# Performance work log

Hardware: AMD Instinct MI355X
Metric: run time of the kernel (lower is better)

The kernel has to match this reference:

```python
import jax, jax.numpy as jnp
import numpy as np

B, N, F_IN, F_OUT = 8, 2048, 128, 128


def setup_inputs() -> dict:
    key = jax.random.key(0)
    k1, k2, k3, k4 = jax.random.split(key, 4)
    h = jax.random.normal(k1, (B, N, F_IN), dtype=jnp.float32)
    adj = (jax.random.uniform(k2, (B, N, N)) > 0.5).astype(jnp.float32)
    adj = jnp.maximum(adj, jnp.eye(N, dtype=jnp.float32)[None])
    # torch nn.Linear weights: W is [out_features, in_features], a is [1, 2*out_features]
    W = jax.random.normal(k3, (F_OUT, F_IN), dtype=jnp.float32) * 0.05
    a = jax.random.normal(k4, (1, 2 * F_OUT), dtype=jnp.float32) * 0.05
    return {"h": h, "adj": adj, "W": W, "a": a}


def reference(h, adj, W, a):
    # Wh = W(h): [B, N, F_OUT]
    Wh = jnp.einsum("bnf,of->bno", h, W)
    # attn_fc(concat(Wh_i, Wh_j)) == (Wh_i @ a1) + (Wh_j @ a2): exact split of the
    # linear layer, avoiding the O(B*N*N*2F) concat intermediate.
    a1 = a[0, :F_OUT]
    a2 = a[0, F_OUT:]
    e_i = Wh @ a1  # [B, N]  score contribution of destination node i
    e_j = Wh @ a2  # [B, N]  score contribution of source node j
    e = e_i[:, :, None] + e_j[:, None, :]  # [B, N, N]
    e = e + (1.0 - adj) * (-1e9)
    alpha = jax.nn.softmax(e, axis=-1)  # [B, N, N]
    # weighted aggregation: h_out[b,i] = sum_j alpha[b,i,j] * Wh[b,j]
    h_out = jnp.einsum("bij,bjo->bio", alpha, Wh)
    return h_out
```

## Files before the change

### kernel.cpp

```cpp
#include <hip/hip_runtime.h>
#include <stdint.h>

#define AS1 __attribute__((address_space(1)))
#define AS3 __attribute__((address_space(3)))

typedef __bf16 bf16x8 __attribute__((ext_vector_type(8)));
typedef float f32x4 __attribute__((ext_vector_type(4)));

constexpr int NB = 8;
constexpr int N  = 2048;
constexpr int F  = 128;
constexpr size_t NSL = (size_t)NB * N * F;
constexpr size_t DSL = (size_t)NB * N;

__device__ __forceinline__ unsigned short bf16r(float f) {
    unsigned u = __float_as_uint(f);
    return (unsigned short)((u + 0x7FFFu + ((u >> 16) & 1u)) >> 16);
}
__device__ __forceinline__ float bf2f(unsigned short s) {
    return __uint_as_float(((unsigned)s) << 16);
}


__global__ __launch_bounds__(256) void k1_wh(const float* __restrict__ h,
                                             const float* __restrict__ W,
                                             const float* __restrict__ a,
                                             unsigned short* __restrict__ Wb2,
                                             unsigned short* __restrict__ p16) {
    __shared__ float epart[2][64];

    const int tid  = threadIdx.x;
    const int lane = tid & 63, wid = tid >> 6;
    const int quad = lane >> 4, l15 = lane & 15;
    const int wm = wid >> 1, wn = wid & 1;
    const int m0 = blockIdx.x * 64;
    const int batch = m0 >> 11;
    const int nbase = m0 & 2047;

    f32x4 acc[2][4] = {};

#pragma unroll
    for (int kk = 0; kk < 4; ++kk) {
        const int k = kk * 32 + quad * 8;
        bf16x8 afr[2], bfr[4];
#pragma unroll
        for (int rt = 0; rt < 2; ++rt) {
            const float* src = h + (size_t)(m0 + wm * 32 + rt * 16 + l15) * F + k;
            float4 x0 = *(const float4*)src;
            float4 x1 = *(const float4*)(src + 4);
            afr[rt][0] = (__bf16)x0.x; afr[rt][1] = (__bf16)x0.y;
            afr[rt][2] = (__bf16)x0.z; afr[rt][3] = (__bf16)x0.w;
            afr[rt][4] = (__bf16)x1.x; afr[rt][5] = (__bf16)x1.y;
            afr[rt][6] = (__bf16)x1.z; afr[rt][7] = (__bf16)x1.w;
        }
#pragma unroll
        for (int ct = 0; ct < 4; ++ct) {
            const int o = wn * 64 + ct * 16 + l15;
            const float* src = W + (size_t)o * F + k;
            float4 x0 = *(const float4*)src;
            float4 x1 = *(const float4*)(src + 4);
            bfr[ct][0] = (__bf16)x0.x; bfr[ct][1] = (__bf16)x0.y;
            bfr[ct][2] = (__bf16)x0.z; bfr[ct][3] = (__bf16)x0.w;
            bfr[ct][4] = (__bf16)x1.x; bfr[ct][5] = (__bf16)x1.y;
            bfr[ct][6] = (__bf16)x1.z; bfr[ct][7] = (__bf16)x1.w;
        }
#pragma unroll
        for (int rt = 0; rt < 2; ++rt)
#pragma unroll
            for (int ct = 0; ct < 4; ++ct)
                acc[rt][ct] = __builtin_amdgcn_mfma_f32_16x16x32_bf16(
                    afr[rt], bfr[ct], acc[rt][ct], 0, 0, 0);
    }

    float a2v[4];
#pragma unroll
    for (int ct = 0; ct < 4; ++ct) a2v[ct] = a[F + wn * 64 + ct * 16 + l15];

    float ep[2][4];
#pragma unroll
    for (int rt = 0; rt < 2; ++rt)
#pragma unroll
        for (int g = 0; g < 4; ++g) {
            float s = 0.f;
#pragma unroll
            for (int ct = 0; ct < 4; ++ct) s += acc[rt][ct][g] * a2v[ct];
            ep[rt][g] = s;
        }
#pragma unroll
    for (int m = 1; m < 16; m <<= 1)
#pragma unroll
        for (int rt = 0; rt < 2; ++rt)
#pragma unroll
            for (int g = 0; g < 4; ++g)
                ep[rt][g] += __shfl_xor(ep[rt][g], m);

    if (l15 == 0)
#pragma unroll
        for (int rt = 0; rt < 2; ++rt)
#pragma unroll
            for (int g = 0; g < 4; ++g)
                epart[wn][wm * 32 + rt * 16 + quad * 4 + g] = ep[rt][g];
    __syncthreads();

#pragma unroll
    for (int rt = 0; rt < 2; ++rt)
#pragma unroll
        for (int ct = 0; ct < 4; ++ct) {
            const int o  = wn * 64 + ct * 16 + l15;
            const int r0 = wm * 32 + rt * 16 + quad * 4;
            const int n0 = nbase + r0;
            ushort4 v;
#pragma unroll
            for (int g = 0; g < 4; ++g) {
                const float e  = epart[0][r0 + g] + epart[1][r0 + g];
                const float pf = bf2f(bf16r(expf(e)));
                (&v.x)[g] = bf16r(pf * acc[rt][ct][g]);
            }
            size_t off = (size_t)batch * N * F + (size_t)(n0 >> 3) * 1024 + o * 8 + (n0 & 7);
            *(ushort4*)&Wb2[off] = v;
        }

    if (tid < 64) {
        const float e = epart[0][tid] + epart[1][tid];
        p16[batch * N + nbase + tid] = bf16r(expf(e));
    }
}

__global__ __launch_bounds__(256) void k3_attn(const float* __restrict__ adj,
                                               const unsigned short* __restrict__ Wb2,
                                               const unsigned short* __restrict__ p16,
                                               unsigned short* __restrict__ nump,
                                               float* __restrict__ denp) {
    __shared__ __align__(16) float          At[2][64 * 32];
    __shared__ __align__(16) unsigned short Bt[2][4 * 1024];
    __shared__ __align__(16) unsigned short Pt[512];

    const int tid  = threadIdx.x;
    const int lane = tid & 63, wid = tid >> 6;
    const int quad = lane >> 4, l15 = lane & 15;
    const int wm = wid >> 1, wn = wid & 1;
    const int b  = blockIdx.x & 7;
    const int r  = blockIdx.x >> 3;
    const int it = r >> 2, jq = r & 3;
    const int i0 = it * 64, j0 = jq * 512;

    const float* aSrcs[2];
#pragma unroll
    for (int s = 0; s < 2; ++s) {
        const int ri = (wid * 2 + s) * 8 + (lane >> 3);
        aSrcs[s] = adj + (size_t)b * N * N + (size_t)(i0 + ri) * N + j0
                 + (((lane & 7) ^ (ri & 7)) << 2);
    }
    const char* bSrc = (const char*)Wb2 + (size_t)b * N * F * 2
                     + (size_t)jq * 131072 + (size_t)wid * 2048 + lane * 16;
    const char* pSrc = (const char*)p16 + ((size_t)b * N + j0) * 2 + lane * 16;

    auto stage = [&](int buf, int c) {
#pragma unroll
        for (int s = 0; s < 2; ++s)
            __builtin_amdgcn_global_load_lds((const AS1 void*)(aSrcs[s] + c * 32),
                (AS3 void*)((char*)&At[buf][0] + (wid * 2 + s) * 1024), 16, 0, 0);
#pragma unroll
        for (int s = 0; s < 2; ++s)
            __builtin_amdgcn_global_load_lds(
                (const AS1 void*)(bSrc + (size_t)c * 8192 + s * 1024),
                (AS3 void*)((char*)&Bt[buf][0] + wid * 2048 + s * 1024), 16, 0, 0);
    };

    f32x4 acc[2][4] = {};
    f32x4 dacc[2] = {};

    if (wid == 0)
        __builtin_amdgcn_global_load_lds((const AS1 void*)pSrc,
            (AS3 void*)((char*)&Pt[0]), 16, 0, 0);
    stage(0, 0);

    for (int c = 0; c < 16; ++c) {
        const int cur = c & 1;
        __syncthreads();
        if (c + 1 < 16) stage(cur ^ 1, c + 1);

        const char* aB = (const char*)&At[cur][0];
        bf16x8 pv = *(const bf16x8*)((const char*)&Pt[0] + c * 64 + quad * 16);

        bf16x8 af[2];
#pragma unroll
        for (int rt = 0; rt < 2; ++rt) {
            const int row = wm * 32 + rt * 16 + l15;
            const int s0 = (quad * 2)     ^ (row & 7);
            const int s1 = (quad * 2 + 1) ^ (row & 7);
            f32x4 x0 = *(const f32x4*)(aB + row * 128 + (s0 << 4));
            f32x4 x1 = *(const f32x4*)(aB + row * 128 + (s1 << 4));
            af[rt][0] = (__bf16)x0[0]; af[rt][1] = (__bf16)x0[1];
            af[rt][2] = (__bf16)x0[2]; af[rt][3] = (__bf16)x0[3];
            af[rt][4] = (__bf16)x1[0]; af[rt][5] = (__bf16)x1[1];
            af[rt][6] = (__bf16)x1[2]; af[rt][7] = (__bf16)x1[3];
        }
#pragma unroll
        for (int ct = 0; ct < 4; ++ct) {
            const char* bb = (const char*)&Bt[cur][0]
                           + quad * 2048 + wn * 1024 + ct * 256 + l15 * 16;
            bf16x8 bf = *(const bf16x8*)bb;
#pragma unroll
            for (int rt = 0; rt < 2; ++rt)
                acc[rt][ct] = __builtin_amdgcn_mfma_f32_16x16x32_bf16(
                    af[rt], bf, acc[rt][ct], 0, 0, 0);
        }
#pragma unroll
        for (int rt = 0; rt < 2; ++rt)
            dacc[rt] = __builtin_amdgcn_mfma_f32_16x16x32_bf16(
                af[rt], pv, dacc[rt], 0, 0, 0);
    }

    unsigned short* np = nump + (size_t)jq * NSL + (size_t)b * N * F;
#pragma unroll
    for (int rt = 0; rt < 2; ++rt)
#pragma unroll
        for (int ct = 0; ct < 4; ++ct) {
            const int o = wn * 64 + ct * 16 + l15;
#pragma unroll
            for (int g = 0; g < 4; ++g) {
                const int i = i0 + wm * 32 + rt * 16 + quad * 4 + g;
                np[(size_t)i * F + o] = bf16r(acc[rt][ct][g]);
            }
        }
    float* dp = denp + (size_t)jq * DSL + (size_t)b * N;
#pragma unroll
    for (int rt = 0; rt < 2; ++rt)
#pragma unroll
        for (int g = 0; g < 4; ++g)
            if (l15 == quad * 4 + g)
                dp[i0 + wm * 32 + rt * 16 + quad * 4 + g] = dacc[rt][g];
}

__global__ __launch_bounds__(256) void k4_reduce(const unsigned short* __restrict__ nump,
                                                 const float* __restrict__ denp,
                                                 float* __restrict__ out) {
    const int b   = blockIdx.x & 7;
    const int row = (blockIdx.x >> 3) * 8 + (threadIdx.x >> 5);
    const int o4  = (threadIdx.x & 31) * 4;
    const size_t base = ((size_t)b * N + row) * F + o4;

    float s0 = 0.f, s1 = 0.f, s2 = 0.f, s3 = 0.f, d = 0.f;
#pragma unroll
    for (int q = 0; q < 4; ++q) {
        ushort4 v = *(const ushort4*)&nump[q * NSL + base];
        s0 += bf2f(v.x); s1 += bf2f(v.y); s2 += bf2f(v.z); s3 += bf2f(v.w);
        d  += denp[q * DSL + (size_t)b * N + row];
    }
    const float inv = 1.0f / d;
    f32x4 o = { s0 * inv, s1 * inv, s2 * inv, s3 * inv };
    *(f32x4*)&out[base] = o;
}

extern "C" void kernel_launch(void* const* d_in, const int* in_sizes, int n_in,
                              void* d_out, int out_size, void* d_ws, size_t ws_size,
                              hipStream_t stream) {
    const float* h   = (const float*)d_in[0];
    const float* adj = (const float*)d_in[1];
    const float* W   = (const float*)d_in[2];
    const float* a   = (const float*)d_in[3];
    float* out = (float*)d_out;

    unsigned short* Wb2  = (unsigned short*)d_ws;
    unsigned short* p16  = (unsigned short*)((char*)d_ws + (4u << 20));
    unsigned short* nump = (unsigned short*)((char*)d_ws + (8u << 20));
    float*          denp = (float*)((char*)d_ws + (24u << 20));

    k1_wh<<<NB * N / 64, 256, 0, stream>>>(h, W, a, Wb2, p16);
    k3_attn<<<NB * 32 * 4, 256, 0, stream>>>(adj, Wb2, p16, nump, denp);
    k4_reduce<<<NB * N / 8, 256, 0, stream>>>(nump, denp, out);
}
```

Before: 221.6 us.

## Fuse attention and reduction into one kernel without split-K partials

Replaces the split-K attention kernel and separate reduction kernel with a single kernel that computes the full j-range per block. It normalizes by the denominator and writes fp32 output directly. Operands now come straight from global memory into registers with one-step software prefetch instead of LDS double buffering. This drops the partial-sum round trip and a launch, but cuts the grid to 512 blocks, lengthens each block's serial loop, and loses LDS reuse of Wb2 tiles across waves.

```diff
diff --git a/kernel.cpp b/kernel.cpp
--- a/kernel.cpp
+++ b/kernel.cpp
@@ -10,8 +10,6 @@
 constexpr int NB = 8;
 constexpr int N  = 2048;
 constexpr int F  = 128;
-constexpr size_t NSL = (size_t)NB * N * F;
-constexpr size_t DSL = (size_t)NB * N;
 
 __device__ __forceinline__ unsigned short bf16r(float f) {
     unsigned u = __float_as_uint(f);
@@ -126,131 +124,73 @@
     }
 }
 
-__global__ __launch_bounds__(256) void k3_attn(const float* __restrict__ adj,
-                                               const unsigned short* __restrict__ Wb2,
-                                               const unsigned short* __restrict__ p16,
-                                               unsigned short* __restrict__ nump,
-                                               float* __restrict__ denp) {
-    __shared__ __align__(16) float          At[2][64 * 32];
-    __shared__ __align__(16) unsigned short Bt[2][4 * 1024];
-    __shared__ __align__(16) unsigned short Pt[512];
-
+__global__ __launch_bounds__(256, 2) void k3_fused(const float* __restrict__ adj,
+                                                   const unsigned short* __restrict__ Wb2,
+                                                   const unsigned short* __restrict__ p16,
+                                                   float* __restrict__ out) {
     const int tid  = threadIdx.x;
     const int lane = tid & 63, wid = tid >> 6;
     const int quad = lane >> 4, l15 = lane & 15;
     const int wm = wid >> 1, wn = wid & 1;
     const int b  = blockIdx.x & 7;
-    const int r  = blockIdx.x >> 3;
-    const int it = r >> 2, jq = r & 3;
-    const int i0 = it * 64, j0 = jq * 512;
-
-    const float* aSrcs[2];
-#pragma unroll
-    for (int s = 0; s < 2; ++s) {
-        const int ri = (wid * 2 + s) * 8 + (lane >> 3);
-        aSrcs[s] = adj + (size_t)b * N * N + (size_t)(i0 + ri) * N + j0
-                 + (((lane & 7) ^ (ri & 7)) << 2);
-    }
-    const char* bSrc = (const char*)Wb2 + (size_t)b * N * F * 2
-                     + (size_t)jq * 131072 + (size_t)wid * 2048 + lane * 16;
-    const char* pSrc = (const char*)p16 + ((size_t)b * N + j0) * 2 + lane * 16;
-
-    auto stage = [&](int buf, int c) {
-#pragma unroll
-        for (int s = 0; s < 2; ++s)
-            __builtin_amdgcn_global_load_lds((const AS1 void*)(aSrcs[s] + c * 32),
-                (AS3 void*)((char*)&At[buf][0] + (wid * 2 + s) * 1024), 16, 0, 0);
-#pragma unroll
-        for (int s = 0; s < 2; ++s)
-            __builtin_amdgcn_global_load_lds(
-                (const AS1 void*)(bSrc + (size_t)c * 8192 + s * 1024),
-                (AS3 void*)((char*)&Bt[buf][0] + wid * 2048 + s * 1024), 16, 0, 0);
-    };
-
-    f32x4 acc[2][4] = {};
-    f32x4 dacc[2] = {};
-
-    if (wid == 0)
-        __builtin_amdgcn_global_load_lds((const AS1 void*)pSrc,
-            (AS3 void*)((char*)&Pt[0]), 16, 0, 0);
-    stage(0, 0);
-
-    for (int c = 0; c < 16; ++c) {
-        const int cur = c & 1;
-        __syncthreads();
-        if (c + 1 < 16) stage(cur ^ 1, c + 1);
-
-        const char* aB = (const char*)&At[cur][0];
-        bf16x8 pv = *(const bf16x8*)((const char*)&Pt[0] + c * 64 + quad * 16);
-
-        bf16x8 af[2];
-#pragma unroll
-        for (int rt = 0; rt < 2; ++rt) {
-            const int row = wm * 32 + rt * 16 + l15;
-            const int s0 = (quad * 2)     ^ (row & 7);
-            const int s1 = (quad * 2 + 1) ^ (row & 7);
-            f32x4 x0 = *(const f32x4*)(aB + row * 128 + (s0 << 4));
-            f32x4 x1 = *(const f32x4*)(aB + row * 128 + (s1 << 4));
-            af[rt][0] = (__bf16)x0[0]; af[rt][1] = (__bf16)x0[1];
-            af[rt][2] = (__bf16)x0[2]; af[rt][3] = (__bf16)x0[3];
-            af[rt][4] = (__bf16)x1[0]; af[rt][5] = (__bf16)x1[1];
-            af[rt][6] = (__bf16)x1[2]; af[rt][7] = (__bf16)x1[3];
-        }
-#pragma unroll
-        for (int ct = 0; ct < 4; ++ct) {
-            const char* bb = (const char*)&Bt[cur][0]
-                           + quad * 2048 + wn * 1024 + ct * 256 + l15 * 16;
-            bf16x8 bf = *(const bf16x8*)bb;
-#pragma unroll
-            for (int rt = 0; rt < 2; ++rt)
-                acc[rt][ct] = __builtin_amdgcn_mfma_f32_16x16x32_bf16(
-                    af[rt], bf, acc[rt][ct], 0, 0, 0);
-        }
-#pragma unroll
-        for (int rt = 0; rt < 2; ++rt)
-            dacc[rt] = __builtin_amdgcn_mfma_f32_16x16x32_bf16(
-                af[rt], pv, dacc[rt], 0, 0, 0);
-    }
-
-    unsigned short* np = nump + (size_t)jq * NSL + (size_t)b * N * F;
-#pragma unroll
-    for (int rt = 0; rt < 2; ++rt)
-#pragma unroll
-        for (int ct = 0; ct < 4; ++ct) {
-            const int o = wn * 64 + ct * 16 + l15;
-#pragma unroll
-            for (int g = 0; g < 4; ++g) {
-                const int i = i0 + wm * 32 + rt * 16 + quad * 4 + g;
-                np[(size_t)i * F + o] = bf16r(acc[rt][ct][g]);
-            }
-        }
-    float* dp = denp + (size_t)jq * DSL + (size_t)b * N;
-#pragma unroll
-    for (int rt = 0; rt < 2; ++rt)
-#pragma unroll
-        for (int g = 0; g < 4; ++g)
-            if (l15 == quad * 4 + g)
-                dp[i0 + wm * 32 + rt * 16 + quad * 4 + g] = dacc[rt][g];
-}
-
-__global__ __launch_bounds__(256) void k4_reduce(const unsigned short* __restrict__ nump,
-                                                 const float* __restrict__ denp,
-                                                 float* __restrict__ out) {
-    const int b   = blockIdx.x & 7;
-    const int row = (blockIdx.x >> 3) * 8 + (threadIdx.x >> 5);
-    const int o4  = (threadIdx.x & 31) * 4;
-    const size_t base = ((size_t)b * N + row) * F + o4;
-
-    float s0 = 0.f, s1 = 0.f, s2 = 0.f, s3 = 0.f, d = 0.f;
-#pragma unroll
-    for (int q = 0; q < 4; ++q) {
-        ushort4 v = *(const ushort4*)&nump[q * NSL + base];
-        s0 += bf2f(v.x); s1 += bf2f(v.y); s2 += bf2f(v.z); s3 += bf2f(v.w);
-        d  += denp[q * DSL + (size_t)b * N + row];
-    }
-    const float inv = 1.0f / d;
-    f32x4 o = { s0 * inv, s1 * inv, s2 * inv, s3 * inv };
-    *(f32x4*)&out[base] = o;
+    const int it = blockIdx.x >> 3;
+    const int i0 = it * 32;
+    const int rowA = i0 + wm * 16 + l15;
+
+    const float* aP = adj + (size_t)b * N * N + (size_t)rowA * N + quad * 8;
+    const char*  bP = (const char*)Wb2 + (size_t)b * (N * F * 2)
+                    + quad * 2048 + wn * 1024 + l15 * 16;
+    const char*  pP = (const char*)p16 + (size_t)b * N * 2 + quad * 16;
+
+    f32x4 acc[4] = {};
+    f32x4 dacc = {0.f, 0.f, 0.f, 0.f};
+
+    f32x4  a0n = *(const f32x4*)(aP);
+    f32x4  a1n = *(const f32x4*)(aP + 4);
+    bf16x8 bn0 = *(const bf16x8*)(bP + 0 * 256);
+    bf16x8 bn1 = *(const bf16x8*)(bP + 1 * 256);
+    bf16x8 bn2 = *(const bf16x8*)(bP + 2 * 256);
+    bf16x8 bn3 = *(const bf16x8*)(bP + 3 * 256);
+    bf16x8 pn  = *(const bf16x8*)(pP);
+
+#pragma unroll 2
+    for (int c = 0; c < 64; ++c) {
+        f32x4  a0 = a0n, a1 = a1n;
+        bf16x8 b0 = bn0, b1 = bn1, b2 = bn2, b3 = bn3, pv = pn;
+        if (c + 1 < 64) {
+            const float* aN = aP + (size_t)(c + 1) * 32;
+            const char*  bN = bP + (size_t)(c + 1) * 8192;
+            a0n = *(const f32x4*)(aN);
+            a1n = *(const f32x4*)(aN + 4);
+            bn0 = *(const bf16x8*)(bN + 0 * 256);
+            bn1 = *(const bf16x8*)(bN + 1 * 256);
+            bn2 = *(const bf16x8*)(bN + 2 * 256);
+            bn3 = *(const bf16x8*)(bN + 3 * 256);
+            pn  = *(const bf16x8*)(pP + (size_t)(c + 1) * 64);
+        }
+        bf16x8 af;
+        af[0] = (__bf16)a0[0]; af[1] = (__bf16)a0[1];
+        af[2] = (__bf16)a0[2]; af[3] = (__bf16)a0[3];
+        af[4] = (__bf16)a1[0]; af[5] = (__bf16)a1[1];
+        af[6] = (__bf16)a1[2]; af[7] = (__bf16)a1[3];
+
+        acc[0] = __builtin_amdgcn_mfma_f32_16x16x32_bf16(af, b0, acc[0], 0, 0, 0);
+        acc[1] = __builtin_amdgcn_mfma_f32_16x16x32_bf16(af, b1, acc[1], 0, 0, 0);
+        acc[2] = __builtin_amdgcn_mfma_f32_16x16x32_bf16(af, b2, acc[2], 0, 0, 0);
+        acc[3] = __builtin_amdgcn_mfma_f32_16x16x32_bf16(af, b3, acc[3], 0, 0, 0);
+        dacc   = __builtin_amdgcn_mfma_f32_16x16x32_bf16(af, pv, dacc,   0, 0, 0);
+    }
+
+#pragma unroll
+    for (int g = 0; g < 4; ++g) {
+        const float inv = 1.0f / dacc[g];
+        float* orow = out + ((size_t)b * N + i0 + wm * 16 + quad * 4 + g) * F
+                    + wn * 64 + l15;
+        orow[0]  = acc[0][g] * inv;
+        orow[16] = acc[1][g] * inv;
+        orow[32] = acc[2][g] * inv;
+        orow[48] = acc[3][g] * inv;
+    }
 }
 
 extern "C" void kernel_launch(void* const* d_in, const int* in_sizes, int n_in,
@@ -262,12 +202,9 @@
     const float* a   = (const float*)d_in[3];
     float* out = (float*)d_out;
 
-    unsigned short* Wb2  = (unsigned short*)d_ws;
-    unsigned short* p16  = (unsigned short*)((char*)d_ws + (4u << 20));
-    unsigned short* nump = (unsigned short*)((char*)d_ws + (8u << 20));
-    float*          denp = (float*)((char*)d_ws + (24u << 20));
+    unsigned short* Wb2 = (unsigned short*)d_ws;
+    unsigned short* p16 = (unsigned short*)((char*)d_ws + (4u << 20));
 
     k1_wh<<<NB * N / 64, 256, 0, stream>>>(h, W, a, Wb2, p16);
-    k3_attn<<<NB * 32 * 4, 256, 0, stream>>>(adj, Wb2, p16, nump, denp);
-    k4_reduce<<<NB * N / 8, 256, 0, stream>>>(nump, denp, out);
-}
+    k3_fused<<<NB * 64, 256, 0, stream>>>(adj, Wb2, p16, out);
+}
```

New measurement: 228.6 us. +3.2%, slower.
